# Optimization experiments

Measured on AMD Instinct MI355X. Metric: run time of the kernel, lower is better.

The kernel has to match this reference:

```python
import jax, jax.numpy as jnp
import numpy as np

BN_EPS = 1e-5
N_NODES = 100000
N_EDGES = 1600000
D = 128


def setup_inputs() -> dict:
    key = jax.random.key(0)
    ks = jax.random.split(key, 8)
    h = jax.random.normal(ks[0], (N_NODES, D), dtype=jnp.float32)
    snorm_n = jax.random.uniform(ks[1], (N_NODES, 1), dtype=jnp.float32)
    eps = jnp.zeros((1,), dtype=jnp.float32)
    W1 = jax.random.normal(ks[2], (D, D), dtype=jnp.float32) * (1.0 / np.sqrt(D))
    b1 = jnp.zeros((D,), dtype=jnp.float32)
    W2 = jax.random.normal(ks[3], (D, D), dtype=jnp.float32) * (1.0 / np.sqrt(D))
    b2 = jnp.zeros((D,), dtype=jnp.float32)
    bn_gamma = jnp.ones((D,), dtype=jnp.float32)
    bn_beta = jnp.zeros((D,), dtype=jnp.float32)
    src = jax.random.randint(ks[4], (N_EDGES,), 0, N_NODES, dtype=jnp.int32)
    dst = jax.random.randint(ks[5], (N_EDGES,), 0, N_NODES, dtype=jnp.int32)
    return {"h": h, "snorm_n": snorm_n, "eps": eps, "W1": W1, "b1": b1,
            "W2": W2, "b2": b2, "bn_gamma": bn_gamma, "bn_beta": bn_beta,
            "src": src, "dst": dst}


def reference(h, snorm_n, eps, W1, b1, W2, b2, bn_gamma, bn_beta, src, dst):
    h_in = h
    # message passing: copy_u + sum reduce -> scatter-add of h[src] into dst
    neigh = jax.ops.segment_sum(h[src], dst, num_segments=N_NODES)  # [N, D]
    x = (1.0 + eps[0]) * h + neigh
    # apply_func: 2-layer MLP (Linear -> ReLU -> Linear)
    x = jax.nn.relu(x @ W1 + b1) @ W2 + b2
    # graph norm w.r.t. graph sizes
    x = x * snorm_n
    # batch norm (training-mode batch statistics over nodes)
    mean = jnp.mean(x, axis=0)
    var = jnp.var(x, axis=0)
    x = (x - mean) * jax.lax.rsqrt(var + BN_EPS) * bn_gamma + bn_beta
    x = jax.nn.relu(x)
    # residual (in_dim == out_dim)
    x = h_in + x
    # dropout p=0.0 -> identity
    return x
```

## Files before the change

### kernel.cpp

```cpp
#include <hip/hip_runtime.h>

#define D 128
#define NN 100000
#define NE 1600000
#define SCAN_NBLK 98
#define GT_ROWS 128
#define GEMM_NT ((NN + GT_ROWS - 1) / GT_ROWS)
#define GEMM_GRID 512
#define NRANGE 8
#define RANGE_SZ 12500
#define STREAM_CAP 204800
#define BINA_GRID 256
#define FILLB_GRID 1024

__global__ void init8_kernel(unsigned int* __restrict__ gcur8)
{
    if (threadIdx.x < NRANGE) gcur8[threadIdx.x] = threadIdx.x * STREAM_CAP;
}

__global__ __launch_bounds__(256) void bin_count_kernel(
    const int* __restrict__ src, const int* __restrict__ dst,
    int* __restrict__ cnt8x, unsigned int* __restrict__ gcur8,
    unsigned int* __restrict__ stream)
{
    __shared__ unsigned int cnt8[NRANGE], base8[NRANGE], off8[NRANGE];
    const int tid = threadIdx.x;
    if (tid < NRANGE) cnt8[tid] = 0;
    __syncthreads();
    int* mycnt = cnt8x + (size_t)(blockIdx.x & 7) * NN;
    const int NT4 = NE / 4;
    for (int i4 = blockIdx.x * 256 + tid; i4 < NT4; i4 += BINA_GRID * 256) {
        int4 d = ((const int4*)dst)[i4];
        atomicAdd(&mycnt[d.x], 1);
        atomicAdd(&mycnt[d.y], 1);
        atomicAdd(&mycnt[d.z], 1);
        atomicAdd(&mycnt[d.w], 1);
        atomicAdd(&cnt8[d.x / RANGE_SZ], 1u);
        atomicAdd(&cnt8[d.y / RANGE_SZ], 1u);
        atomicAdd(&cnt8[d.z / RANGE_SZ], 1u);
        atomicAdd(&cnt8[d.w / RANGE_SZ], 1u);
    }
    __syncthreads();
    if (tid < NRANGE) {
        base8[tid] = atomicAdd(&gcur8[tid], cnt8[tid]);
        off8[tid]  = 0;
    }
    __syncthreads();
    for (int i4 = blockIdx.x * 256 + tid; i4 < NT4; i4 += BINA_GRID * 256) {
        int4 d = ((const int4*)dst)[i4];
        int4 s = ((const int4*)src)[i4];
        {
            int r = d.x / RANGE_SZ; unsigned dl = (unsigned)(d.x - r * RANGE_SZ);
            unsigned pos = base8[r] + atomicAdd(&off8[r], 1u);
            stream[pos] = (dl << 17) | (unsigned)s.x;
        }
        {
            int r = d.y / RANGE_SZ; unsigned dl = (unsigned)(d.y - r * RANGE_SZ);
            unsigned pos = base8[r] + atomicAdd(&off8[r], 1u);
            stream[pos] = (dl << 17) | (unsigned)s.y;
        }
        {
            int r = d.z / RANGE_SZ; unsigned dl = (unsigned)(d.z - r * RANGE_SZ);
            unsigned pos = base8[r] + atomicAdd(&off8[r], 1u);
            stream[pos] = (dl << 17) | (unsigned)s.z;
        }
        {
            int r = d.w / RANGE_SZ; unsigned dl = (unsigned)(d.w - r * RANGE_SZ);
            unsigned pos = base8[r] + atomicAdd(&off8[r], 1u);
            stream[pos] = (dl << 17) | (unsigned)s.w;
        }
    }
}

__global__ __launch_bounds__(256) void scan_local_kernel(
    const int* __restrict__ cnt8x, int* __restrict__ pre, int* __restrict__ blkSum)
{
    __shared__ int lds[256];
    const int t = threadIdx.x;
    const int base = blockIdx.x * 1024 + t * 4;
    int4 v = {0, 0, 0, 0};
    if (base + 3 < NN) {
#pragma unroll
        for (int r = 0; r < NRANGE; ++r) {
            int4 c = *(const int4*)&cnt8x[(size_t)r * NN + base];
            v.x += c.x; v.y += c.y; v.z += c.z; v.w += c.w;
        }
    } else {
#pragma unroll
        for (int r = 0; r < NRANGE; ++r) {
            if (base + 0 < NN) v.x += cnt8x[(size_t)r * NN + base + 0];
            if (base + 1 < NN) v.y += cnt8x[(size_t)r * NN + base + 1];
            if (base + 2 < NN) v.z += cnt8x[(size_t)r * NN + base + 2];
            if (base + 3 < NN) v.w += cnt8x[(size_t)r * NN + base + 3];
        }
    }
    const int s = v.x + v.y + v.z + v.w;
    lds[t] = s;
    __syncthreads();
    for (int off = 1; off < 256; off <<= 1) {
        int val = 0;
        if (t >= off) val = lds[t - off];
        __syncthreads();
        if (t >= off) lds[t] += val;
        __syncthreads();
    }
    const int excl = lds[t] - s;
    if (t == 255) blkSum[blockIdx.x] = lds[255];
    int4 o;
    o.x = excl;
    o.y = excl + v.x;
    o.z = excl + v.x + v.y;
    o.w = excl + v.x + v.y + v.z;
    if (base + 3 < NN) *(int4*)&pre[base] = o;
    else {
        if (base + 0 < NN) pre[base + 0] = o.x;
        if (base + 1 < NN) pre[base + 1] = o.y;
        if (base + 2 < NN) pre[base + 2] = o.z;
        if (base + 3 < NN) pre[base + 3] = o.w;
    }
}

__global__ __launch_bounds__(128) void scan_blk_kernel(
    const int* __restrict__ blkSum, int* __restrict__ blkOfs)
{
    __shared__ int lds[128];
    const int t = threadIdx.x;
    int s = (t < SCAN_NBLK) ? blkSum[t] : 0;
    lds[t] = s;
    __syncthreads();
    for (int off = 1; off < 128; off <<= 1) {
        int val = 0;
        if (t >= off) val = lds[t - off];
        __syncthreads();
        if (t >= off) lds[t] += val;
        __syncthreads();
    }
    blkOfs[t] = lds[t] - s;
}

__global__ __launch_bounds__(256) void scan_finish_kernel(
    const int* __restrict__ pre, const int* __restrict__ blkOfs,
    int* __restrict__ row_start, int* __restrict__ cursor)
{
    int n = blockIdx.x * 256 + threadIdx.x;
    if (n > NN) return;
    int v = (n == NN) ? NE : pre[n] + blkOfs[n >> 10];
    row_start[n] = v;
    if (n < NN) cursor[n] = v;
}

__global__ __launch_bounds__(256) void fill_kernel(
    const unsigned int* __restrict__ stream, const unsigned int* __restrict__ gcur8,
    int* __restrict__ cursor, int* __restrict__ eidx)
{
    const int r = blockIdx.x & 7;
    const int chunk = blockIdx.x >> 3;
    const unsigned s1 = gcur8[r];
    const unsigned stride = (FILLB_GRID / 8) * 256;
    for (unsigned i = (unsigned)r * STREAM_CAP + chunk * 256 + threadIdx.x;
         i < s1; i += stride) {
        unsigned p = stream[i];
        int s  = (int)(p & 0x1FFFFu);
        int dn = r * RANGE_SZ + (int)(p >> 17);
        int pos = atomicAdd(&cursor[dn], 1);
        eidx[pos] = s;
    }
}

__global__ __launch_bounds__(256) void gather_kernel(
    const float* __restrict__ h, const int* __restrict__ row_start,
    const int* __restrict__ eidx, const float* __restrict__ epsp,
    float* __restrict__ x)
{
    int gid  = blockIdx.x * 256 + threadIdx.x;
    int node = gid >> 5;
    int lane = gid & 31;
    if (node >= NN) return;
    const int s0 = row_start[node];
    const int s1 = row_start[node + 1];
    const float sc = 1.0f + epsp[0];
    float4 hv = ((const float4*)(h + (size_t)node * D))[lane];
    float ax = sc * hv.x, ay = sc * hv.y, az = sc * hv.z, aw = sc * hv.w;
    float bx = 0.f, by = 0.f, bz = 0.f, bw = 0.f;
    int e = s0;
    for (; e + 1 < s1; e += 2) {
        int sa = eidx[e];
        int sb = eidx[e + 1];
        float4 va = ((const float4*)(h + (size_t)sa * D))[lane];
        float4 vb = ((const float4*)(h + (size_t)sb * D))[lane];
        ax += va.x; ay += va.y; az += va.z; aw += va.w;
        bx += vb.x; by += vb.y; bz += vb.z; bw += vb.w;
    }
    if (e < s1) {
        int sa = eidx[e];
        float4 va = ((const float4*)(h + (size_t)sa * D))[lane];
        ax += va.x; ay += va.y; az += va.z; aw += va.w;
    }
    float4 o = {ax + bx, ay + by, az + bz, aw + bw};
    ((float4*)(x + (size_t)node * D))[lane] = o;
}

template <int MODE>
__global__ __launch_bounds__(256, 2) void gemm_kernel(
    const float* __restrict__ xin, const float* __restrict__ W,
    const float* __restrict__ bias, const float* __restrict__ snorm,
    float* __restrict__ out, double* __restrict__ stats)
{
    __shared__ float wl[64 * D];
    __shared__ float xb[64 * D];
    const int tid = threadIdx.x;
    const int cg = tid & 15;
    const int rg = tid >> 4;
    const int ca = cg * 4;
    const int cb = 64 + cg * 4;

    float4 bva = ((const float4*)bias)[cg];
    float4 bvb = ((const float4*)bias)[16 + cg];

    float ssum[8], ssq[8];
#pragma unroll
    for (int j = 0; j < 8; ++j) { ssum[j] = 0.f; ssq[j] = 0.f; }

    float4 xs[8], wsg[8];
    auto LOADG = [&](int t, int hh) {
        const int row0 = t * GT_ROWS;
#pragma unroll
        for (int i = 0; i < 8; ++i) {
            int idx = tid + i * 256;
            int row = idx >> 4;
            int kc  = idx & 15;
            int grow = row0 + row;
            xs[i] = (grow < NN)
                ? ((const float4*)(xin + (size_t)grow * D))[hh * 16 + kc]
                : make_float4(0.f, 0.f, 0.f, 0.f);
        }
#pragma unroll
        for (int i = 0; i < 8; ++i) {
            int idx = tid + i * 256;
            int k  = idx >> 5;
            int c4 = idx & 31;
            wsg[i] = ((const float4*)(W + (size_t)(hh * 64 + k) * D))[c4];
        }
    };
    auto WRITEL = [&]() {
#pragma unroll
        for (int i = 0; i < 8; ++i) {
            int idx = tid + i * 256;
            int row = idx >> 4;
            int kc  = idx & 15;
            float v[4] = {xs[i].x, xs[i].y, xs[i].z, xs[i].w};
#pragma unroll
            for (int j = 0; j < 4; ++j)
                xb[(kc * 4 + j) * D + (row ^ (kc << 2))] = v[j];
        }
#pragma unroll
        for (int i = 0; i < 8; ++i) {
            int idx = tid + i * 256;
            int k  = idx >> 5;
            int c4 = idx & 31;
            *(float4*)&wl[k * D + c4 * 4] = wsg[i];
        }
    };

    bool first = true;
    for (int t = blockIdx.x; t < GEMM_NT; t += GEMM_GRID) {
        float acc[8][8];
#pragma unroll
        for (int i = 0; i < 8; ++i)
#pragma unroll
            for (int j = 0; j < 8; ++j) acc[i][j] = 0.f;

#pragma unroll 1
        for (int hh = 0; hh < 2; ++hh) {
            if (first) { LOADG(t, 0); first = false; }
            __syncthreads();
            WRITEL();
            int nt = (hh == 0) ? t : t + GEMM_GRID;
            int nh = hh ^ 1;
            if (nt < GEMM_NT) LOADG(nt, nh);
            __syncthreads();

#pragma unroll 8
            for (int k = 0; k < 64; ++k) {
                const int V = ((k >> 2) & 15) << 2;
                float4 xa = *(const float4*)&xb[k * D + ((rg * 8) ^ V)];
                float4 xc = *(const float4*)&xb[k * D + ((rg * 8 + 4) ^ V)];
                float4 wa = *(const float4*)&wl[k * D + ca];
                float4 wb = *(const float4*)&wl[k * D + cb];
                float xr[8] = {xa.x, xa.y, xa.z, xa.w, xc.x, xc.y, xc.z, xc.w};
                float wr[8] = {wa.x, wa.y, wa.z, wa.w, wb.x, wb.y, wb.z, wb.w};
#pragma unroll
                for (int i = 0; i < 8; ++i)
#pragma unroll
                    for (int j = 0; j < 8; ++j)
                        acc[i][j] = fmaf(xr[i], wr[j], acc[i][j]);
            }
        }

#pragma unroll
        for (int i = 0; i < 8; ++i) {
            int row = t * GT_ROWS + rg * 8 + i;
            if (row < NN) {
                float oa[4], ob[4];
                if (MODE == 1) {
                    oa[0] = fmaxf(acc[i][0] + bva.x, 0.f);
                    oa[1] = fmaxf(acc[i][1] + bva.y, 0.f);
                    oa[2] = fmaxf(acc[i][2] + bva.z, 0.f);
                    oa[3] = fmaxf(acc[i][3] + bva.w, 0.f);
                    ob[0] = fmaxf(acc[i][4] + bvb.x, 0.f);
                    ob[1] = fmaxf(acc[i][5] + bvb.y, 0.f);
                    ob[2] = fmaxf(acc[i][6] + bvb.z, 0.f);
                    ob[3] = fmaxf(acc[i][7] + bvb.w, 0.f);
                } else {
                    const float sn = snorm[row];
                    oa[0] = (acc[i][0] + bva.x) * sn;
                    oa[1] = (acc[i][1] + bva.y) * sn;
                    oa[2] = (acc[i][2] + bva.z) * sn;
                    oa[3] = (acc[i][3] + bva.w) * sn;
                    ob[0] = (acc[i][4] + bvb.x) * sn;
                    ob[1] = (acc[i][5] + bvb.y) * sn;
                    ob[2] = (acc[i][6] + bvb.z) * sn;
                    ob[3] = (acc[i][7] + bvb.w) * sn;
#pragma unroll
                    for (int j = 0; j < 4; ++j) {
                        ssum[j]     += oa[j];  ssq[j]     += oa[j] * oa[j];
                        ssum[4 + j] += ob[j];  ssq[4 + j] += ob[j] * ob[j];
                    }
                }
                float* op = out + (size_t)row * D;
                *(float4*)&op[ca] = *(float4*)&oa[0];
                *(float4*)&op[cb] = *(float4*)&ob[0];
            }
        }
    }

    if (MODE == 2) {
        float* red = xb;
        __syncthreads();
#pragma unroll
        for (int j = 0; j < 4; ++j) {
            red[rg * D + ca + j] = ssum[j];
            red[rg * D + cb + j] = ssum[4 + j];
        }
        __syncthreads();
        if (tid < D) {
            float s = 0.f;
#pragma unroll
            for (int r = 0; r < 16; ++r) s += red[r * D + tid];
            atomicAdd(&stats[tid], (double)s);
        }
        __syncthreads();
#pragma unroll
        for (int j = 0; j < 4; ++j) {
            red[rg * D + ca + j] = ssq[j];
            red[rg * D + cb + j] = ssq[4 + j];
        }
        __syncthreads();
        if (tid < D) {
            float s = 0.f;
#pragma unroll
            for (int r = 0; r < 16; ++r) s += red[r * D + tid];
            atomicAdd(&stats[D + tid], (double)s);
        }
    }
}

__global__ void bn_prep_kernel(const double* __restrict__ stats,
                               const float* __restrict__ gamma,
                               const float* __restrict__ beta,
                               float* __restrict__ sc_sh)
{
    int c = threadIdx.x;
    double mean = stats[c] * (1.0 / NN);
    double var  = stats[D + c] * (1.0 / NN) - mean * mean;
    float rs = rsqrtf((float)var + 1e-5f);
    float sc = gamma[c] * rs;
    sc_sh[c]     = sc;
    sc_sh[D + c] = beta[c] - (float)mean * sc;
}

__global__ __launch_bounds__(256) void finalize_kernel(
    const float* __restrict__ y, const float* __restrict__ h,
    const float* __restrict__ sc_sh, float* __restrict__ out)
{
    int i  = blockIdx.x * 256 + threadIdx.x;
    int cf = i & 31;
    float4 yv = ((const float4*)y)[i];
    float4 hv = ((const float4*)h)[i];
    float4 sc = ((const float4*)sc_sh)[cf];
    float4 sh = ((const float4*)(sc_sh + D))[cf];
    float4 o;
    o.x = hv.x + fmaxf(fmaf(yv.x, sc.x, sh.x), 0.0f);
    o.y = hv.y + fmaxf(fmaf(yv.y, sc.y, sh.y), 0.0f);
    o.z = hv.z + fmaxf(fmaf(yv.z, sc.z, sh.z), 0.0f);
    o.w = hv.w + fmaxf(fmaf(yv.w, sc.w, sh.w), 0.0f);
    ((float4*)out)[i] = o;
}

extern "C" void kernel_launch(void* const* d_in, const int* in_sizes, int n_in,
                              void* d_out, int out_size, void* d_ws, size_t ws_size,
                              hipStream_t stream)
{
    const float* h     = (const float*)d_in[0];
    const float* snorm = (const float*)d_in[1];
    const float* eps   = (const float*)d_in[2];
    const float* W1    = (const float*)d_in[3];
    const float* b1    = (const float*)d_in[4];
    const float* W2    = (const float*)d_in[5];
    const float* b2    = (const float*)d_in[6];
    const float* gamma = (const float*)d_in[7];
    const float* beta  = (const float*)d_in[8];
    const int*   src   = (const int*)d_in[9];
    const int*   dst   = (const int*)d_in[10];
    float* out = (float*)d_out;

    char* ws = (char*)d_ws;
    const size_t BUF_BYTES = (size_t)NN * D * sizeof(float);
    float*  buf       = (float*)ws;
    double* stats     = (double*)(ws + BUF_BYTES);
    float*  sc_sh     = (float*)(ws + BUF_BYTES + 2048);
    char*   p         = ws + BUF_BYTES + 4096;
    int*    pre       = (int*)p;            p += (size_t)NN * 4;
    int*    row_start = (int*)p;            p += (size_t)(NN + 4) * 4;
    int*    cursor    = (int*)p;            p += (size_t)NN * 4;
    int*    blkSum    = (int*)p;            p += 512;
    int*    blkOfs    = (int*)p;            p += 512;
    unsigned int* gcur8  = (unsigned int*)p;  p += 256;
    int*    eidx      = (int*)p;            p += (size_t)NE * 4;
    unsigned int* stream8 = (unsigned int*)p;
    int*    cnt8x     = eidx;

    hipMemsetAsync(cnt8x, 0, (size_t)NRANGE * NN * 4, stream);
    hipMemsetAsync(stats, 0, 2048, stream);
    init8_kernel<<<1, 64, 0, stream>>>(gcur8);

    bin_count_kernel<<<BINA_GRID, 256, 0, stream>>>(src, dst, cnt8x, gcur8, stream8);
    scan_local_kernel<<<SCAN_NBLK, 256, 0, stream>>>(cnt8x, pre, blkSum);
    scan_blk_kernel<<<1, 128, 0, stream>>>(blkSum, blkOfs);
    scan_finish_kernel<<<(NN + 256) / 256 + 1, 256, 0, stream>>>(pre, blkOfs, row_start, cursor);
    fill_kernel<<<FILLB_GRID, 256, 0, stream>>>(stream8, gcur8, cursor, eidx);

    gather_kernel<<<NN * 32 / 256, 256, 0, stream>>>(h, row_start, eidx, eps, buf);

    gemm_kernel<1><<<GEMM_GRID, 256, 0, stream>>>(buf, W1, b1, nullptr, buf, nullptr);
    gemm_kernel<2><<<GEMM_GRID, 256, 0, stream>>>(buf, W2, b2, snorm, buf, stats);

    bn_prep_kernel<<<1, D, 0, stream>>>(stats, gamma, beta, sc_sh);
    finalize_kernel<<<NN * D / 4 / 256, 256, 0, stream>>>(buf, h, sc_sh, out);
}
```

Baseline: 532.4 us.

## Fuse both MLP GEMMs into one kernel keeping hidden activations in LDS

Replaces the two separate GEMM launches with one fused kernel. For each 64-row tile it computes Linear1+ReLU, writes the hidden result back into shared memory in the transposed swizzled layout, then runs Linear2 with snorm scaling and the BN statistics. This removes one full round trip of the 100000x128 intermediate through global memory and one launch. In exchange each tile is half as tall, so every weight tile is reloaded per row tile more often and there are more barriers per tile, which lowers arithmetic intensity per weight load.

```diff
diff --git a/kernel.cpp b/kernel.cpp
--- a/kernel.cpp
+++ b/kernel.cpp
@@ -4,9 +4,9 @@
 #define NN 100000
 #define NE 1600000
 #define SCAN_NBLK 98
-#define GT_ROWS 128
-#define GEMM_NT ((NN + GT_ROWS - 1) / GT_ROWS)
-#define GEMM_GRID 512
+#define MT_ROWS 64
+#define MLP_NT ((NN + MT_ROWS - 1) / MT_ROWS)
+#define MLP_GRID 512
 #define NRANGE 8
 #define RANGE_SZ 12500
 #define STREAM_CAP 204800
@@ -200,59 +200,66 @@
     ((float4*)(x + (size_t)node * D))[lane] = o;
 }
 
-template <int MODE>
-__global__ __launch_bounds__(256, 2) void gemm_kernel(
-    const float* __restrict__ xin, const float* __restrict__ W,
-    const float* __restrict__ bias, const float* __restrict__ snorm,
+__global__ __launch_bounds__(256, 2) void fused_mlp_kernel(
+    const float* __restrict__ xin, const float* __restrict__ W1,
+    const float* __restrict__ b1, const float* __restrict__ W2,
+    const float* __restrict__ b2, const float* __restrict__ snorm,
     float* __restrict__ out, double* __restrict__ stats)
 {
+    __shared__ float xb[MT_ROWS * D];
     __shared__ float wl[64 * D];
-    __shared__ float xb[64 * D];
     const int tid = threadIdx.x;
     const int cg = tid & 15;
     const int rg = tid >> 4;
     const int ca = cg * 4;
     const int cb = 64 + cg * 4;
 
-    float4 bva = ((const float4*)bias)[cg];
-    float4 bvb = ((const float4*)bias)[16 + cg];
+    float4 b1a = ((const float4*)b1)[cg];
+    float4 b1b = ((const float4*)b1)[16 + cg];
+    float4 b2a = ((const float4*)b2)[cg];
+    float4 b2b = ((const float4*)b2)[16 + cg];
 
     float ssum[8], ssq[8];
 #pragma unroll
     for (int j = 0; j < 8; ++j) { ssum[j] = 0.f; ssq[j] = 0.f; }
 
     float4 xs[8], wsg[8];
-    auto LOADG = [&](int t, int hh) {
-        const int row0 = t * GT_ROWS;
+    auto LOADX = [&](int t) {
+        const int row0 = t * MT_ROWS;
 #pragma unroll
         for (int i = 0; i < 8; ++i) {
             int idx = tid + i * 256;
-            int row = idx >> 4;
-            int kc  = idx & 15;
+            int row = idx >> 5;
+            int kc  = idx & 31;
             int grow = row0 + row;
             xs[i] = (grow < NN)
-                ? ((const float4*)(xin + (size_t)grow * D))[hh * 16 + kc]
+                ? ((const float4*)xin)[(size_t)grow * 32 + kc]
                 : make_float4(0.f, 0.f, 0.f, 0.f);
         }
+    };
+    auto WRITEX = [&]() {
+#pragma unroll
+        for (int i = 0; i < 8; ++i) {
+            int idx = tid + i * 256;
+            int row = idx >> 5;
+            int kc  = idx & 31;
+            int V   = (kc & 15) << 2;
+            float v[4] = {xs[i].x, xs[i].y, xs[i].z, xs[i].w};
+#pragma unroll
+            for (int j = 0; j < 4; ++j)
+                xb[(kc * 4 + j) * MT_ROWS + (row ^ V)] = v[j];
+        }
+    };
+    auto LOADW = [&](const float* Wp, int hh) {
 #pragma unroll
         for (int i = 0; i < 8; ++i) {
             int idx = tid + i * 256;
             int k  = idx >> 5;
             int c4 = idx & 31;
-            wsg[i] = ((const float4*)(W + (size_t)(hh * 64 + k) * D))[c4];
+            wsg[i] = ((const float4*)Wp)[(size_t)(hh * 64 + k) * 32 + c4];
         }
     };
-    auto WRITEL = [&]() {
-#pragma unroll
-        for (int i = 0; i < 8; ++i) {
-            int idx = tid + i * 256;
-            int row = idx >> 4;
-            int kc  = idx & 15;
-            float v[4] = {xs[i].x, xs[i].y, xs[i].z, xs[i].w};
-#pragma unroll
-            for (int j = 0; j < 4; ++j)
-                xb[(kc * 4 + j) * D + (row ^ (kc << 2))] = v[j];
-        }
+    auto WRITEW = [&]() {
 #pragma unroll
         for (int i = 0; i < 8; ++i) {
             int idx = tid + i * 256;
@@ -262,106 +269,134 @@
         }
     };
 
+    float acc[4][8];
+    auto KLOOP = [&](int hh) {
+#pragma unroll 8
+        for (int kk = 0; kk < 64; ++kk) {
+            const int kg = hh * 64 + kk;
+            const int V  = ((kg >> 2) & 15) << 2;
+            float4 xa = *(const float4*)&xb[kg * MT_ROWS + ((rg * 4) ^ V)];
+            float4 wa = *(const float4*)&wl[kk * D + ca];
+            float4 wb = *(const float4*)&wl[kk * D + cb];
+            float xr[4] = {xa.x, xa.y, xa.z, xa.w};
+            float wr[8] = {wa.x, wa.y, wa.z, wa.w, wb.x, wb.y, wb.z, wb.w};
+#pragma unroll
+            for (int i = 0; i < 4; ++i)
+#pragma unroll
+                for (int j = 0; j < 8; ++j)
+                    acc[i][j] = fmaf(xr[i], wr[j], acc[i][j]);
+        }
+    };
+
     bool first = true;
-    for (int t = blockIdx.x; t < GEMM_NT; t += GEMM_GRID) {
-        float acc[8][8];
-#pragma unroll
-        for (int i = 0; i < 8; ++i)
+    for (int t = blockIdx.x; t < MLP_NT; t += MLP_GRID) {
+        if (first) {
+            LOADX(t);
+            __syncthreads();
+            WRITEX();
+            LOADW(W1, 0);
+            first = false;
+        }
+        WRITEW();
+        LOADW(W1, 1);
+        __syncthreads();
+#pragma unroll
+        for (int i = 0; i < 4; ++i)
 #pragma unroll
             for (int j = 0; j < 8; ++j) acc[i][j] = 0.f;
-
-#pragma unroll 1
-        for (int hh = 0; hh < 2; ++hh) {
-            if (first) { LOADG(t, 0); first = false; }
-            __syncthreads();
-            WRITEL();
-            int nt = (hh == 0) ? t : t + GEMM_GRID;
-            int nh = hh ^ 1;
-            if (nt < GEMM_NT) LOADG(nt, nh);
-            __syncthreads();
-
-#pragma unroll 8
-            for (int k = 0; k < 64; ++k) {
-                const int V = ((k >> 2) & 15) << 2;
-                float4 xa = *(const float4*)&xb[k * D + ((rg * 8) ^ V)];
-                float4 xc = *(const float4*)&xb[k * D + ((rg * 8 + 4) ^ V)];
-                float4 wa = *(const float4*)&wl[k * D + ca];
-                float4 wb = *(const float4*)&wl[k * D + cb];
-                float xr[8] = {xa.x, xa.y, xa.z, xa.w, xc.x, xc.y, xc.z, xc.w};
-                float wr[8] = {wa.x, wa.y, wa.z, wa.w, wb.x, wb.y, wb.z, wb.w};
-#pragma unroll
-                for (int i = 0; i < 8; ++i)
-#pragma unroll
-                    for (int j = 0; j < 8; ++j)
-                        acc[i][j] = fmaf(xr[i], wr[j], acc[i][j]);
+        KLOOP(0);
+        __syncthreads();
+        WRITEW();
+        LOADW(W2, 0);
+        __syncthreads();
+        KLOOP(1);
+
+        __syncthreads();
+        {
+#pragma unroll
+            for (int j = 0; j < 4; ++j) {
+                int c0 = ca + j, c1 = cb + j;
+                float ba0 = (&b1a.x)[j], bb0 = (&b1b.x)[j];
+                float4 v0, v1;
+                (&v0.x)[0] = fmaxf(acc[0][j] + ba0, 0.f);
+                (&v0.x)[1] = fmaxf(acc[1][j] + ba0, 0.f);
+                (&v0.x)[2] = fmaxf(acc[2][j] + ba0, 0.f);
+                (&v0.x)[3] = fmaxf(acc[3][j] + ba0, 0.f);
+                (&v1.x)[0] = fmaxf(acc[0][4 + j] + bb0, 0.f);
+                (&v1.x)[1] = fmaxf(acc[1][4 + j] + bb0, 0.f);
+                (&v1.x)[2] = fmaxf(acc[2][4 + j] + bb0, 0.f);
+                (&v1.x)[3] = fmaxf(acc[3][4 + j] + bb0, 0.f);
+                int V0 = ((c0 >> 2) & 15) << 2;
+                int V1 = ((c1 >> 2) & 15) << 2;
+                *(float4*)&xb[c0 * MT_ROWS + ((rg * 4) ^ V0)] = v0;
+                *(float4*)&xb[c1 * MT_ROWS + ((rg * 4) ^ V1)] = v1;
             }
         }
-
-#pragma unroll
-        for (int i = 0; i < 8; ++i) {
-            int row = t * GT_ROWS + rg * 8 + i;
+        WRITEW();
+        LOADW(W2, 1);
+        __syncthreads();
+
+#pragma unroll
+        for (int i = 0; i < 4; ++i)
+#pragma unroll
+            for (int j = 0; j < 8; ++j) acc[i][j] = 0.f;
+        KLOOP(0);
+        __syncthreads();
+        WRITEW();
+        int tn = t + MLP_GRID;
+        if (tn < MLP_NT) LOADX(tn);
+        __syncthreads();
+        KLOOP(1);
+
+#pragma unroll
+        for (int i = 0; i < 4; ++i) {
+            int row = t * MT_ROWS + rg * 4 + i;
             if (row < NN) {
+                const float sn = snorm[row];
                 float oa[4], ob[4];
-                if (MODE == 1) {
-                    oa[0] = fmaxf(acc[i][0] + bva.x, 0.f);
-                    oa[1] = fmaxf(acc[i][1] + bva.y, 0.f);
-                    oa[2] = fmaxf(acc[i][2] + bva.z, 0.f);
-                    oa[3] = fmaxf(acc[i][3] + bva.w, 0.f);
-                    ob[0] = fmaxf(acc[i][4] + bvb.x, 0.f);
-                    ob[1] = fmaxf(acc[i][5] + bvb.y, 0.f);
-                    ob[2] = fmaxf(acc[i][6] + bvb.z, 0.f);
-                    ob[3] = fmaxf(acc[i][7] + bvb.w, 0.f);
-                } else {
-                    const float sn = snorm[row];
-                    oa[0] = (acc[i][0] + bva.x) * sn;
-                    oa[1] = (acc[i][1] + bva.y) * sn;
-                    oa[2] = (acc[i][2] + bva.z) * sn;
-                    oa[3] = (acc[i][3] + bva.w) * sn;
-                    ob[0] = (acc[i][4] + bvb.x) * sn;
-                    ob[1] = (acc[i][5] + bvb.y) * sn;
-                    ob[2] = (acc[i][6] + bvb.z) * sn;
-                    ob[3] = (acc[i][7] + bvb.w) * sn;
-#pragma unroll
-                    for (int j = 0; j < 4; ++j) {
-                        ssum[j]     += oa[j];  ssq[j]     += oa[j] * oa[j];
-                        ssum[4 + j] += ob[j];  ssq[4 + j] += ob[j] * ob[j];
-                    }
+#pragma unroll
+                for (int j = 0; j < 4; ++j) {
+                    oa[j] = (acc[i][j] + (&b2a.x)[j]) * sn;
+                    ob[j] = (acc[i][4 + j] + (&b2b.x)[j]) * sn;
+                    ssum[j]     += oa[j];  ssq[j]     += oa[j] * oa[j];
+                    ssum[4 + j] += ob[j];  ssq[4 + j] += ob[j] * ob[j];
                 }
                 float* op = out + (size_t)row * D;
                 *(float4*)&op[ca] = *(float4*)&oa[0];
                 *(float4*)&op[cb] = *(float4*)&ob[0];
             }
         }
-    }
-
-    if (MODE == 2) {
-        float* red = xb;
-        __syncthreads();
-#pragma unroll
-        for (int j = 0; j < 4; ++j) {
-            red[rg * D + ca + j] = ssum[j];
-            red[rg * D + cb + j] = ssum[4 + j];
-        }
-        __syncthreads();
-        if (tid < D) {
-            float s = 0.f;
-#pragma unroll
-            for (int r = 0; r < 16; ++r) s += red[r * D + tid];
-            atomicAdd(&stats[tid], (double)s);
-        }
-        __syncthreads();
-#pragma unroll
-        for (int j = 0; j < 4; ++j) {
-            red[rg * D + ca + j] = ssq[j];
-            red[rg * D + cb + j] = ssq[4 + j];
-        }
-        __syncthreads();
-        if (tid < D) {
-            float s = 0.f;
-#pragma unroll
-            for (int r = 0; r < 16; ++r) s += red[r * D + tid];
-            atomicAdd(&stats[D + tid], (double)s);
-        }
+        __syncthreads();
+        if (tn < MLP_NT) WRITEX();
+        LOADW(W1, 0);
+    }
+
+    float* red = xb;
+    __syncthreads();
+#pragma unroll
+    for (int j = 0; j < 4; ++j) {
+        red[rg * D + ca + j] = ssum[j];
+        red[rg * D + cb + j] = ssum[4 + j];
+    }
+    __syncthreads();
+    if (tid < D) {
+        float s = 0.f;
+#pragma unroll
+        for (int r = 0; r < 16; ++r) s += red[r * D + tid];
+        atomicAdd(&stats[tid], (double)s);
+    }
+    __syncthreads();
+#pragma unroll
+    for (int j = 0; j < 4; ++j) {
+        red[rg * D + ca + j] = ssq[j];
+        red[rg * D + cb + j] = ssq[4 + j];
+    }
+    __syncthreads();
+    if (tid < D) {
+        float s = 0.f;
+#pragma unroll
+        for (int r = 0; r < 16; ++r) s += red[r * D + tid];
+        atomicAdd(&stats[D + tid], (double)s);
     }
 }
 
@@ -442,8 +477,7 @@
 
     gather_kernel<<<NN * 32 / 256, 256, 0, stream>>>(h, row_start, eidx, eps, buf);
 
-    gemm_kernel<1><<<GEMM_GRID, 256, 0, stream>>>(buf, W1, b1, nullptr, buf, nullptr);
-    gemm_kernel<2><<<GEMM_GRID, 256, 0, stream>>>(buf, W2, b2, snorm, buf, stats);
+    fused_mlp_kernel<<<MLP_GRID, 256, 0, stream>>>(buf, W1, b1, W2, b2, snorm, buf, stats);
 
     bn_prep_kernel<<<1, D, 0, stream>>>(stats, gamma, beta, sc_sh);
     finalize_kernel<<<NN * D / 4 / 256, 256, 0, stream>>>(buf, h, sc_sh, out);
```

Result: slower. 549.2 us (+3.2%).
